# Kernel optimization log

Measured on AMD Instinct MI355X. Metric: run time of the kernel, lower is better.

## Reference

```python
import jax, jax.numpy as jnp
import numpy as np
import math

D = 2048
H = 32
HKV = 8
HD = D // H
ROPE_BASE = 10000.0


def _rope_cache(T, hd, base=ROPE_BASE):
    theta = 1.0 / base ** (jnp.arange(0, hd, 2, dtype=jnp.float32) / hd)  # [hd//2]
    t = jnp.arange(T, dtype=jnp.float32)
    freqs = t[:, None] * theta[None, :]  # [T, hd//2]
    return jnp.cos(freqs), jnp.sin(freqs)


def _apply_rope(x, cos, sin):
    # x: [B, H, T, HD]; interleaved-pair rotation
    B, Hh, T, hd = x.shape
    x_ = x.reshape(B, Hh, T, hd // 2, 2)
    x1, x2 = x_[..., 0], x_[..., 1]
    c = cos[None, None, :, :]
    s = sin[None, None, :, :]
    rx1 = x1 * c - x2 * s
    rx2 = x1 * s + x2 * c
    return jnp.stack([rx1, rx2], axis=-1).reshape(B, Hh, T, hd)


def setup_inputs() -> dict:
    key = jax.random.key(0)
    ks = jax.random.split(key, 5)
    B, T = 1, 2048
    sc = 0.02
    return {
        "x": jax.random.normal(ks[0], (B, T, D), dtype=jnp.float32),
        "wq": jax.random.normal(ks[1], (D, D), dtype=jnp.float32) * sc,
        "wk": jax.random.normal(ks[2], (HKV * HD, D), dtype=jnp.float32) * sc,
        "wv": jax.random.normal(ks[3], (HKV * HD, D), dtype=jnp.float32) * sc,
        "wo": jax.random.normal(ks[4], (D, D), dtype=jnp.float32) * sc,
    }


def reference(x, wq, wk, wv, wo):
    B, T, _ = x.shape
    q = (x @ wq.T).reshape(B, T, H, HD).transpose(0, 2, 1, 3)      # [B,H,T,HD]
    k = (x @ wk.T).reshape(B, T, HKV, HD).transpose(0, 2, 1, 3)    # [B,HKV,T,HD]
    v = (x @ wv.T).reshape(B, T, HKV, HD).transpose(0, 2, 1, 3)

    cos, sin = _rope_cache(T, HD)
    q = _apply_rope(q, cos, sin)
    k = _apply_rope(k, cos, sin)

    rep = H // HKV
    k = jnp.repeat(k, rep, axis=1)  # repeat_interleave over head dim
    v = jnp.repeat(v, rep, axis=1)

    scores = jnp.einsum("bhtd,bhsd->bhts", q, k) / math.sqrt(HD)
    mask = jnp.triu(jnp.full((T, T), -jnp.inf, dtype=scores.dtype), k=1)
    scores = scores + mask[None, None, :, :]
    attn = jax.nn.softmax(scores, axis=-1)

    y = jnp.einsum("bhts,bhsd->bhtd", attn, v)
    y = y.transpose(0, 2, 1, 3).reshape(B, T, D)
    return y @ wo.T
```

## Files before the change

### kernel.cpp

```cpp
#include <hip/hip_runtime.h>
#include <hip/hip_bf16.h>
#include <cstdint>
#include <cstddef>

#define TT 2048
#define DDIM 2048
#define NH 32
#define NKV 8
#define HDIM 64

typedef __attribute__((ext_vector_type(8))) short bf16x8;
typedef __attribute__((ext_vector_type(4))) float f32x4;
typedef __attribute__((ext_vector_type(16))) float f32x16;

__device__ __forceinline__ unsigned short f2bf(float f) {
  unsigned u = __float_as_uint(f);
  unsigned r = 0x7FFFu + ((u >> 16) & 1u);
  return (unsigned short)((u + r) >> 16);
}
__device__ __forceinline__ float bf2f(unsigned short u) {
  return __uint_as_float((unsigned)u << 16);
}

__device__ __forceinline__ void gl_lds16(const void* g, void* l) {
  __builtin_amdgcn_global_load_lds(
      (const __attribute__((address_space(1))) void*)g,
      (__attribute__((address_space(3))) void*)l, 16, 0, 0);
}

__device__ __forceinline__ unsigned pkbf(float lo, float hi) {
  unsigned r;
  asm("v_cvt_pk_bf16_f32 %0, %1, %2" : "=v"(r) : "v"(lo), "v"(hi));
  return r;
}
__device__ __forceinline__ void swap32(unsigned& dst, unsigned& src) {
  asm volatile("v_permlane32_swap_b32 %0, %1" : "+v"(dst), "+v"(src));
}
union W4 { unsigned w[4]; bf16x8 v; };

__global__ __launch_bounds__(256)
void cast5_kernel(const float* __restrict__ x, const float* __restrict__ wq,
                  const float* __restrict__ wk, const float* __restrict__ wv,
                  const float* __restrict__ wo,
                  unsigned short* __restrict__ xb, unsigned short* __restrict__ wqb,
                  unsigned short* __restrict__ wkb, unsigned short* __restrict__ wvb,
                  unsigned short* __restrict__ wob) {
  int i = blockIdx.x * 256 + threadIdx.x;
  const float* s; unsigned short* d; int off;
  if (i < 1048576)      { s = x;  d = xb;  off = i; }
  else if (i < 2097152) { s = wq; d = wqb; off = i - 1048576; }
  else if (i < 2359296) { s = wk; d = wkb; off = i - 2097152; }
  else if (i < 2621440) { s = wv; d = wvb; off = i - 2359296; }
  else                  { s = wo; d = wob; off = i - 2621440; }
  float4 f = reinterpret_cast<const float4*>(s)[off];
  ushort4 o;
  o.x = f2bf(f.x); o.y = f2bf(f.y); o.z = f2bf(f.z); o.w = f2bf(f.w);
  reinterpret_cast<ushort4*>(d)[off] = o;
}

__device__ __forceinline__ void gemm64_body(
    const unsigned short* __restrict__ A, const unsigned short* __restrict__ B,
    int K, size_t arow, size_t brow,
    unsigned short (*As)[64 * 64], unsigned short (*Bs)[128 * 64],
    f32x4 (&acc)[2][4]) {
  const int tid = threadIdx.x;
  const int wave = tid >> 6, lane = tid & 63;
  const int wm = wave >> 1, wn = wave & 1;
  const int lr = lane & 15;
  const int gb = lane >> 4;
  const int srow = lane >> 3;
  const int scol = (((lane & 7) ^ srow) << 3);

#define G64_STAGE(buf, k0)                                                       \
  {                                                                              \
    for (int i = 0; i < 2; ++i) {                                                \
      int blk = wave * 2 + i;                                                    \
      int r = blk * 8 + srow;                                                    \
      gl_lds16(A + arow + (size_t)r * K + (k0) + scol, &As[buf][blk * 8 * 64]);  \
    }                                                                            \
    for (int i = 0; i < 4; ++i) {                                                \
      int blk = wave * 4 + i;                                                    \
      int r = blk * 8 + srow;                                                    \
      gl_lds16(B + brow + (size_t)r * K + (k0) + scol, &Bs[buf][blk * 8 * 64]);  \
    }                                                                            \
  }

  const int nt = K >> 6;
  G64_STAGE(0, 0)
  __syncthreads();
  int cur = 0;
  for (int t = 0; t < nt; ++t) {
    if (t + 1 < nt) { G64_STAGE(cur ^ 1, (t + 1) << 6) }

    bf16x8 af[2][2], bfr[2][4];
    for (int mi = 0; mi < 2; ++mi) {
      int row = wm * 32 + mi * 16 + lr, sw = row & 7;
      af[0][mi] = *reinterpret_cast<const bf16x8*>(&As[cur][row * 64 + ((gb ^ sw) << 3)]);
      af[1][mi] = *reinterpret_cast<const bf16x8*>(&As[cur][row * 64 + (((4 + gb) ^ sw) << 3)]);
    }
    for (int ni = 0; ni < 4; ++ni) {
      int row = wn * 64 + ni * 16 + lr, sw = row & 7;
      bfr[0][ni] = *reinterpret_cast<const bf16x8*>(&Bs[cur][row * 64 + ((gb ^ sw) << 3)]);
      bfr[1][ni] = *reinterpret_cast<const bf16x8*>(&Bs[cur][row * 64 + (((4 + gb) ^ sw) << 3)]);
    }
    __builtin_amdgcn_s_setprio(1);
    for (int kk = 0; kk < 2; ++kk)
      for (int mi = 0; mi < 2; ++mi)
        for (int ni = 0; ni < 4; ++ni)
          acc[mi][ni] = __builtin_amdgcn_mfma_f32_16x16x32_bf16(af[kk][mi], bfr[kk][ni], acc[mi][ni], 0, 0, 0);
    __builtin_amdgcn_s_setprio(0);
    __syncthreads();
    cur ^= 1;
  }
#undef G64_STAGE
}

__global__ __launch_bounds__(256, 3)
void qkv_fused_kernel(const unsigned short* __restrict__ xb,
                      const unsigned short* __restrict__ wqb,
                      const unsigned short* __restrict__ wkb,
                      const unsigned short* __restrict__ wvb,
                      unsigned short* __restrict__ qhb,
                      unsigned short* __restrict__ khb,
                      unsigned short* __restrict__ vtb) {
  __shared__ __align__(16) unsigned short As[2][64 * 64];
  __shared__ __align__(16) unsigned short Bs[2][128 * 64];
  const int l = (int)(blockIdx.y * gridDim.x + blockIdx.x);
  const int nl = (l & 7) * 96 + (l >> 3);
  const int bx = nl & 31;
  const int bn = nl >> 5;

  const unsigned short* B; int n0, mode;
  if (bn < 16)      { B = wqb; n0 = bn;      mode = 0; }
  else if (bn < 20) { B = wkb; n0 = bn - 16; mode = 1; }
  else              { B = wvb; n0 = bn - 20; mode = 2; }

  f32x4 acc[2][4];
  for (int i = 0; i < 2; ++i)
    for (int j = 0; j < 4; ++j)
      acc[i][j] = (f32x4){0.f, 0.f, 0.f, 0.f};

  gemm64_body(xb, B, 2048, (size_t)(bx * 64) * 2048,
              (size_t)(n0 * 128) * 2048, As, Bs, acc);

  const int tid = threadIdx.x;
  const int wave = tid >> 6, lane = tid & 63;
  const int wm = wave >> 1, wn = wave & 1;
  const int lr = lane & 15;

  if (mode == 2) {
#pragma unroll
    for (int mi = 0; mi < 2; ++mi)
#pragma unroll
      for (int ni = 0; ni < 4; ++ni) {
        int n = n0 * 128 + wn * 64 + ni * 16 + lr;
        int tb = bx * 64 + wm * 32 + mi * 16 + (lane >> 4) * 4;
        ushort4 u;
        u.x = f2bf(acc[mi][ni][0]); u.y = f2bf(acc[mi][ni][1]);
        u.z = f2bf(acc[mi][ni][2]); u.w = f2bf(acc[mi][ni][3]);
        *reinterpret_cast<ushort4*>(&vtb[(size_t)n * TT + tb]) = u;
      }
  } else {
    unsigned short* dst = (mode == 0) ? qhb : khb;
    const float scale = (mode == 0) ? 0.125f : 1.0f;
#pragma unroll
    for (int mi = 0; mi < 2; ++mi)
#pragma unroll
      for (int ni = 0; ni < 4; ++ni) {
        int n = n0 * 128 + wn * 64 + ni * 16 + lr;
        int hh = n >> 6, d = n & 63, ii = d >> 1;
        float theta = exp2f(-(float)(2 * ii) * (13.287712379549449f / 64.0f));
        int tb = bx * 64 + wm * 32 + mi * 16 + (lane >> 4) * 4;
#pragma unroll
        for (int r = 0; r < 4; ++r) {
          float self = acc[mi][ni][r];
          float part = __shfl_xor(self, 1);
          float sn, cs;
          __sincosf((float)(tb + r) * theta, &sn, &cs);
          float val = (d & 1) ? (part * sn + self * cs) : (self * cs - part * sn);
          dst[((size_t)hh * TT + tb + r) * HDIM + d] = f2bf(val * scale);
        }
      }
  }
}

__global__ __launch_bounds__(256, 3)
void out_gemm_kernel(const unsigned short* __restrict__ yb,
                     const unsigned short* __restrict__ wob,
                     float* __restrict__ out) {
  __shared__ __align__(16) unsigned short As[2][64 * 64];
  __shared__ __align__(16) unsigned short Bs[2][128 * 64];
  const int l = (int)(blockIdx.y * gridDim.x + blockIdx.x);
  const int nl = (l & 7) * 64 + (l >> 3);
  const int bx = nl & 31;
  const int by = nl >> 5;

  f32x4 acc[2][4];
  for (int i = 0; i < 2; ++i)
    for (int j = 0; j < 4; ++j)
      acc[i][j] = (f32x4){0.f, 0.f, 0.f, 0.f};

  gemm64_body(yb, wob, 2048, (size_t)(bx * 64) * 2048,
              (size_t)(by * 128) * 2048, As, Bs, acc);

  const int tid = threadIdx.x;
  const int wave = tid >> 6, lane = tid & 63;
  const int wm = wave >> 1, wn = wave & 1;
  const int lr = lane & 15;
#pragma unroll
  for (int mi = 0; mi < 2; ++mi)
#pragma unroll
    for (int ni = 0; ni < 4; ++ni) {
      int col = by * 128 + wn * 64 + ni * 16 + lr;
      int rbase = bx * 64 + wm * 32 + mi * 16 + (lane >> 4) * 4;
#pragma unroll
      for (int r = 0; r < 4; ++r)
        out[(size_t)(rbase + r) * DDIM + col] = acc[mi][ni][r];
    }
}

__global__ __launch_bounds__(256)
void attn_kernel(const unsigned short* __restrict__ qh,
                 const unsigned short* __restrict__ kh,
                 const unsigned short* __restrict__ vt,
                 unsigned short* __restrict__ po,
                 float* __restrict__ pl) {
  __shared__ __align__(16) unsigned short Ks[2][64 * 64];
  __shared__ __align__(16) unsigned short Vts[2][64 * 64];
  const int kvg = blockIdx.x;
  const int by = blockIdx.y;
  const int qt = 63 - (by >> 1);
  const int par = by & 1;
  const int tid = threadIdx.x, wave = tid >> 6, lane = tid & 63;
  const int h = kvg * 4 + wave;
  const int qc = lane & 31, hi = lane >> 5;
  const int srow = lane >> 3;
  const int scol = (((lane & 7) ^ srow) << 3);

  bf16x8 qa[4];
  {
    const unsigned short* qrow = qh + ((size_t)h * TT + qt * 32 + qc) * HDIM + hi * 8;
#pragma unroll
    for (int ks = 0; ks < 4; ++ks)
      qa[ks] = *reinterpret_cast<const bf16x8*>(qrow + ks * 16);
  }

  f32x16 oA, oB;
#pragma unroll
  for (int r = 0; r < 16; ++r) { oA[r] = 0.f; oB[r] = 0.f; }
  float l_r = 0.f;

  const int njb = (qt >> 1) + 1;
  const int cnt = (njb - par + 1) >> 1;

#define A_STAGE(buf, jbx) do {                                                        \
    for (int i = 0; i < 2; ++i) {                                                     \
      int rblk = wave * 2 + i;                                                        \
      int rr = rblk * 8 + srow;                                                       \
      gl_lds16(kh + ((size_t)kvg * TT + (size_t)(jbx) * 64 + rr) * HDIM + scol,       \
               &Ks[buf][rblk * 8 * 64]);                                              \
      gl_lds16(vt + ((size_t)(kvg * HDIM + rr)) * TT + (size_t)(jbx) * 64 + scol,     \
               &Vts[buf][rblk * 8 * 64]);                                             \
    } } while (0)

  if (cnt > 0) {
    A_STAGE(0, par);
    __syncthreads();
    int cur = 0;

    for (int it = 0; it < cnt; ++it) {
      const int jb = par + 2 * it;
      if (it + 1 < cnt) A_STAGE(cur ^ 1, jb + 2);
      const bool diag = (jb == njb - 1);
      const bool hasB = (!diag) || (qt & 1);

      f32x16 stA, stB;
#pragma unroll
      for (int r = 0; r < 16; ++r) { stA[r] = 0.f; stB[r] = 0.f; }
      __builtin_amdgcn_s_setprio(1);
#pragma unroll
      for (int ks = 0; ks < 4; ++ks) {
        int row = qc, g = 2 * ks + hi;
        bf16x8 kf = *reinterpret_cast<const bf16x8*>(&Ks[cur][row * 64 + ((g ^ (row & 7)) << 3)]);
        stA = __builtin_amdgcn_mfma_f32_32x32x16_bf16(kf, qa[ks], stA, 0, 0, 0);
      }
      if (hasB) {
#pragma unroll
        for (int ks = 0; ks < 4; ++ks) {
          int row = 32 + qc, g = 2 * ks + hi;
          bf16x8 kf = *reinterpret_cast<const bf16x8*>(&Ks[cur][row * 64 + ((g ^ (row & 7)) << 3)]);
          stB = __builtin_amdgcn_mfma_f32_32x32x16_bf16(kf, qa[ks], stB, 0, 0, 0);
        }
      }
      __builtin_amdgcn_s_setprio(0);

      if (diag) {
        if (qt & 1) {
#pragma unroll
          for (int r = 0; r < 16; ++r) {
            int jloc = (r & 3) + 8 * (r >> 2) + 4 * hi;
            stB[r] = (jloc > qc) ? -1e30f : stB[r];
          }
        } else {
#pragma unroll
          for (int r = 0; r < 16; ++r) {
            int jloc = (r & 3) + 8 * (r >> 2) + 4 * hi;
            stA[r] = (jloc > qc) ? -1e30f : stA[r];
          }
        }
      }

#pragma unroll
      for (int r = 0; r < 16; ++r) { stA[r] = __expf(stA[r]); l_r += stA[r]; }
      if (hasB) {
#pragma unroll
        for (int r = 0; r < 16; ++r) { stB[r] = __expf(stB[r]); l_r += stB[r]; }
      }

      W4 pf0, pf1, pf2, pf3;
#define REPACK(F0, F1, S)                                                   \
      F0.w[0] = pkbf(S[0], S[1]);  F0.w[1] = pkbf(S[2], S[3]);              \
      F0.w[2] = pkbf(S[4], S[5]);  F0.w[3] = pkbf(S[6], S[7]);              \
      swap32(F0.w[0], F0.w[2]);    swap32(F0.w[1], F0.w[3]);                \
      F1.w[0] = pkbf(S[8], S[9]);  F1.w[1] = pkbf(S[10], S[11]);            \
      F1.w[2] = pkbf(S[12], S[13]); F1.w[3] = pkbf(S[14], S[15]);           \
      swap32(F1.w[0], F1.w[2]);    swap32(F1.w[1], F1.w[3]);
      REPACK(pf0, pf1, stA)
      if (hasB) { REPACK(pf2, pf3, stB) }
#undef REPACK

      {
        const unsigned short* Vb = &Vts[cur][0];
        int r0 = qc, r1 = 32 + qc;
        int s0 = r0 & 7, s1 = r1 & 7;
        bf16x8 b;
        __builtin_amdgcn_s_setprio(1);
        b = *reinterpret_cast<const bf16x8*>(Vb + r0 * 64 + (((0 + hi) ^ s0) << 3));
        oA = __builtin_amdgcn_mfma_f32_32x32x16_bf16(pf0.v, b, oA, 0, 0, 0);
        b = *reinterpret_cast<const bf16x8*>(Vb + r1 * 64 + (((0 + hi) ^ s1) << 3));
        oB = __builtin_amdgcn_mfma_f32_32x32x16_bf16(pf0.v, b, oB, 0, 0, 0);
        b = *reinterpret_cast<const bf16x8*>(Vb + r0 * 64 + (((2 + hi) ^ s0) << 3));
        oA = __builtin_amdgcn_mfma_f32_32x32x16_bf16(pf1.v, b, oA, 0, 0, 0);
        b = *reinterpret_cast<const bf16x8*>(Vb + r1 * 64 + (((2 + hi) ^ s1) << 3));
        oB = __builtin_amdgcn_mfma_f32_32x32x16_bf16(pf1.v, b, oB, 0, 0, 0);
        if (hasB) {
          b = *reinterpret_cast<const bf16x8*>(Vb + r0 * 64 + (((4 + hi) ^ s0) << 3));
          oA = __builtin_amdgcn_mfma_f32_32x32x16_bf16(pf2.v, b, oA, 0, 0, 0);
          b = *reinterpret_cast<const bf16x8*>(Vb + r1 * 64 + (((4 + hi) ^ s1) << 3));
          oB = __builtin_amdgcn_mfma_f32_32x32x16_bf16(pf2.v, b, oB, 0, 0, 0);
          b = *reinterpret_cast<const bf16x8*>(Vb + r0 * 64 + (((6 + hi) ^ s0) << 3));
          oA = __builtin_amdgcn_mfma_f32_32x32x16_bf16(pf3.v, b, oA, 0, 0, 0);
          b = *reinterpret_cast<const bf16x8*>(Vb + r1 * 64 + (((6 + hi) ^ s1) << 3));
          oB = __builtin_amdgcn_mfma_f32_32x32x16_bf16(pf3.v, b, oB, 0, 0, 0);
        }
        __builtin_amdgcn_s_setprio(0);
      }
      __syncthreads();
      cur ^= 1;
    }
  }
#undef A_STAGE

  l_r += __shfl_xor(l_r, 32);

  unsigned short* pop = po + (size_t)par * ((size_t)NH * TT * HDIM);
#pragma unroll
  for (int r = 0; r < 16; ++r) {
    int qrow = (r & 3) + 8 * (r >> 2) + 4 * hi;
    size_t base = ((size_t)h * TT + qt * 32 + qrow) * HDIM + qc;
    pop[base] = f2bf(oA[r]);
    pop[base + 32] = f2bf(oB[r]);
  }
  if (hi == 0) {
    size_t idx = ((size_t)par * NH + h) * TT + qt * 32 + qc;
    pl[idx] = l_r;
  }
}

__global__ __launch_bounds__(256)
void attn_merge_kernel(const unsigned short* __restrict__ po,
                       const float* __restrict__ pl,
                       unsigned short* __restrict__ y) {
  int idx = blockIdx.x * 256 + threadIdx.x;
  int row = idx >> 4;
  int d0 = (idx & 15) << 2;
  int h = row >> 11, t = row & (TT - 1);
  const size_t P = (size_t)NH * TT * HDIM;
  const int NT = NH * TT;

  float l0 = pl[row], l1 = pl[NT + row];
  ushort4 u0 = *reinterpret_cast<const ushort4*>(&po[(size_t)row * HDIM + d0]);
  ushort4 u1 = *reinterpret_cast<const ushort4*>(&po[P + (size_t)row * HDIM + d0]);
  float inv = 1.0f / (l0 + l1);
  ushort4 o;
  o.x = f2bf((bf2f(u0.x) + bf2f(u1.x)) * inv);
  o.y = f2bf((bf2f(u0.y) + bf2f(u1.y)) * inv);
  o.z = f2bf((bf2f(u0.z) + bf2f(u1.z)) * inv);
  o.w = f2bf((bf2f(u0.w) + bf2f(u1.w)) * inv);
  *reinterpret_cast<ushort4*>(&y[(size_t)t * DDIM + h * HDIM + d0]) = o;
}

extern "C" void kernel_launch(void* const* d_in, const int* in_sizes, int n_in,
                              void* d_out, int out_size, void* d_ws, size_t ws_size,
                              hipStream_t stream) {
  const float* x  = (const float*)d_in[0];
  const float* wq = (const float*)d_in[1];
  const float* wk = (const float*)d_in[2];
  const float* wv = (const float*)d_in[3];
  const float* wo = (const float*)d_in[4];
  float* out = (float*)d_out;
  char* ws = (char*)d_ws;

  unsigned short* xb  = (unsigned short*)(ws + (size_t)0);
  unsigned short* wqb = (unsigned short*)(ws + ((size_t)8  << 20));
  unsigned short* wkb = (unsigned short*)(ws + ((size_t)16 << 20));
  unsigned short* wvb = (unsigned short*)(ws + ((size_t)18 << 20));
  unsigned short* wob = (unsigned short*)(ws + ((size_t)20 << 20));
  unsigned short* po  = (unsigned short*)(ws + ((size_t)28 << 20));
  float*          pl  = (float*)(ws + ((size_t)45 << 20));
  unsigned short* qhb = (unsigned short*)(ws + ((size_t)52 << 20));
  unsigned short* khb = (unsigned short*)(ws + ((size_t)60 << 20));
  unsigned short* vtb = (unsigned short*)(ws + ((size_t)62 << 20));
  unsigned short* yb  = (unsigned short*)(ws + ((size_t)64 << 20));

  cast5_kernel<<<14336, 256, 0, stream>>>(x, wq, wk, wv, wo, xb, wqb, wkb, wvb, wob);

  qkv_fused_kernel<<<dim3(32, 24), 256, 0, stream>>>(xb, wqb, wkb, wvb, qhb, khb, vtb);

  attn_kernel<<<dim3(8, 128), 256, 0, stream>>>(qhb, khb, vtb, po, pl);
  attn_merge_kernel<<<4096, 256, 0, stream>>>(po, pl, yb);

  out_gemm_kernel<<<dim3(32, 16), 256, 0, stream>>>(yb, wob, out);
}
```

Measured before the change: 115.6 us.

## Fuse weight fp32-to-bf16 conversion into GEMM B-tile loading

The weight casts are removed from the standalone cast pass. The GEMMs now load fp32 weight tiles into registers, convert them to bf16 with packed conversion instructions, and store them to LDS after the MFMA work, so the next tile is still prefetched. This drops the separate write and re-read of the bf16 weights. In exchange, each GEMM block re-reads fp32 weights at twice the bytes (each B tile is read by 32 row-blocks), and register pressure rises from the staged float4s.

```diff
diff --git a/kernel.cpp b/kernel.cpp
--- a/kernel.cpp
+++ b/kernel.cpp
@@ -39,27 +39,16 @@
 union W4 { unsigned w[4]; bf16x8 v; };
 
 __global__ __launch_bounds__(256)
-void cast5_kernel(const float* __restrict__ x, const float* __restrict__ wq,
-                  const float* __restrict__ wk, const float* __restrict__ wv,
-                  const float* __restrict__ wo,
-                  unsigned short* __restrict__ xb, unsigned short* __restrict__ wqb,
-                  unsigned short* __restrict__ wkb, unsigned short* __restrict__ wvb,
-                  unsigned short* __restrict__ wob) {
+void cast_x_kernel(const float* __restrict__ x, unsigned short* __restrict__ xb) {
   int i = blockIdx.x * 256 + threadIdx.x;
-  const float* s; unsigned short* d; int off;
-  if (i < 1048576)      { s = x;  d = xb;  off = i; }
-  else if (i < 2097152) { s = wq; d = wqb; off = i - 1048576; }
-  else if (i < 2359296) { s = wk; d = wkb; off = i - 2097152; }
-  else if (i < 2621440) { s = wv; d = wvb; off = i - 2359296; }
-  else                  { s = wo; d = wob; off = i - 2621440; }
-  float4 f = reinterpret_cast<const float4*>(s)[off];
+  float4 f = reinterpret_cast<const float4*>(x)[i];
   ushort4 o;
   o.x = f2bf(f.x); o.y = f2bf(f.y); o.z = f2bf(f.z); o.w = f2bf(f.w);
-  reinterpret_cast<ushort4*>(d)[off] = o;
-}
-
-__device__ __forceinline__ void gemm64_body(
-    const unsigned short* __restrict__ A, const unsigned short* __restrict__ B,
+  reinterpret_cast<ushort4*>(xb)[i] = o;
+}
+
+__device__ __forceinline__ void gemm64f_body(
+    const unsigned short* __restrict__ A, const float* __restrict__ B,
     int K, size_t arow, size_t brow,
     unsigned short (*As)[64 * 64], unsigned short (*Bs)[128 * 64],
     f32x4 (&acc)[2][4]) {
@@ -70,27 +59,44 @@
   const int gb = lane >> 4;
   const int srow = lane >> 3;
   const int scol = (((lane & 7) ^ srow) << 3);
-
-#define G64_STAGE(buf, k0)                                                       \
-  {                                                                              \
-    for (int i = 0; i < 2; ++i) {                                                \
-      int blk = wave * 2 + i;                                                    \
-      int r = blk * 8 + srow;                                                    \
-      gl_lds16(A + arow + (size_t)r * K + (k0) + scol, &As[buf][blk * 8 * 64]);  \
-    }                                                                            \
-    for (int i = 0; i < 4; ++i) {                                                \
-      int blk = wave * 4 + i;                                                    \
-      int r = blk * 8 + srow;                                                    \
-      gl_lds16(B + brow + (size_t)r * K + (k0) + scol, &Bs[buf][blk * 8 * 64]);  \
-    }                                                                            \
+  const int bcol = (lane & 7) << 3;
+  const int bdst = srow * 64 + scol;
+
+  float4 breg[4][2];
+
+#define A_STG(buf, k0)                                                         \
+  for (int i = 0; i < 2; ++i) {                                                \
+    int blk = wave * 2 + i;                                                    \
+    int r = blk * 8 + srow;                                                    \
+    gl_lds16(A + arow + (size_t)r * K + (k0) + scol, &As[buf][blk * 8 * 64]);  \
+  }
+#define B_LOAD(k0)                                                             \
+  for (int i = 0; i < 4; ++i) {                                                \
+    int blk = wave * 4 + i;                                                    \
+    int r = blk * 8 + srow;                                                    \
+    const float* p = B + brow + (size_t)r * K + (k0) + bcol;                   \
+    breg[i][0] = *reinterpret_cast<const float4*>(p);                          \
+    breg[i][1] = *reinterpret_cast<const float4*>(p + 4);                      \
+  }
+#define B_STORE(buf)                                                           \
+  for (int i = 0; i < 4; ++i) {                                                \
+    int blk = wave * 4 + i;                                                    \
+    W4 w;                                                                      \
+    w.w[0] = pkbf(breg[i][0].x, breg[i][0].y);                                 \
+    w.w[1] = pkbf(breg[i][0].z, breg[i][0].w);                                 \
+    w.w[2] = pkbf(breg[i][1].x, breg[i][1].y);                                 \
+    w.w[3] = pkbf(breg[i][1].z, breg[i][1].w);                                 \
+    *reinterpret_cast<bf16x8*>(&Bs[buf][blk * 512 + bdst]) = w.v;              \
   }
 
   const int nt = K >> 6;
-  G64_STAGE(0, 0)
+  B_LOAD(0)
+  A_STG(0, 0)
+  B_STORE(0)
   __syncthreads();
   int cur = 0;
   for (int t = 0; t < nt; ++t) {
-    if (t + 1 < nt) { G64_STAGE(cur ^ 1, (t + 1) << 6) }
+    if (t + 1 < nt) { B_LOAD((t + 1) << 6) A_STG(cur ^ 1, (t + 1) << 6) }
 
     bf16x8 af[2][2], bfr[2][4];
     for (int mi = 0; mi < 2; ++mi) {
@@ -109,17 +115,20 @@
         for (int ni = 0; ni < 4; ++ni)
           acc[mi][ni] = __builtin_amdgcn_mfma_f32_16x16x32_bf16(af[kk][mi], bfr[kk][ni], acc[mi][ni], 0, 0, 0);
     __builtin_amdgcn_s_setprio(0);
+    if (t + 1 < nt) { B_STORE(cur ^ 1) }
     __syncthreads();
     cur ^= 1;
   }
-#undef G64_STAGE
+#undef A_STG
+#undef B_LOAD
+#undef B_STORE
 }
 
 __global__ __launch_bounds__(256, 3)
 void qkv_fused_kernel(const unsigned short* __restrict__ xb,
-                      const unsigned short* __restrict__ wqb,
-                      const unsigned short* __restrict__ wkb,
-                      const unsigned short* __restrict__ wvb,
+                      const float* __restrict__ wq,
+                      const float* __restrict__ wk,
+                      const float* __restrict__ wv,
                       unsigned short* __restrict__ qhb,
                       unsigned short* __restrict__ khb,
                       unsigned short* __restrict__ vtb) {
@@ -130,18 +139,18 @@
   const int bx = nl & 31;
   const int bn = nl >> 5;
 
-  const unsigned short* B; int n0, mode;
-  if (bn < 16)      { B = wqb; n0 = bn;      mode = 0; }
-  else if (bn < 20) { B = wkb; n0 = bn - 16; mode = 1; }
-  else              { B = wvb; n0 = bn - 20; mode = 2; }
+  const float* B; int n0, mode;
+  if (bn < 16)      { B = wq; n0 = bn;      mode = 0; }
+  else if (bn < 20) { B = wk; n0 = bn - 16; mode = 1; }
+  else              { B = wv; n0 = bn - 20; mode = 2; }
 
   f32x4 acc[2][4];
   for (int i = 0; i < 2; ++i)
     for (int j = 0; j < 4; ++j)
       acc[i][j] = (f32x4){0.f, 0.f, 0.f, 0.f};
 
-  gemm64_body(xb, B, 2048, (size_t)(bx * 64) * 2048,
-              (size_t)(n0 * 128) * 2048, As, Bs, acc);
+  gemm64f_body(xb, B, 2048, (size_t)(bx * 64) * 2048,
+               (size_t)(n0 * 128) * 2048, As, Bs, acc);
 
   const int tid = threadIdx.x;
   const int wave = tid >> 6, lane = tid & 63;
@@ -186,7 +195,7 @@
 
 __global__ __launch_bounds__(256, 3)
 void out_gemm_kernel(const unsigned short* __restrict__ yb,
-                     const unsigned short* __restrict__ wob,
+                     const float* __restrict__ wo,
                      float* __restrict__ out) {
   __shared__ __align__(16) unsigned short As[2][64 * 64];
   __shared__ __align__(16) unsigned short Bs[2][128 * 64];
@@ -200,8 +209,8 @@
     for (int j = 0; j < 4; ++j)
       acc[i][j] = (f32x4){0.f, 0.f, 0.f, 0.f};
 
-  gemm64_body(yb, wob, 2048, (size_t)(bx * 64) * 2048,
-              (size_t)(by * 128) * 2048, As, Bs, acc);
+  gemm64f_body(yb, wo, 2048, (size_t)(bx * 64) * 2048,
+               (size_t)(by * 128) * 2048, As, Bs, acc);
 
   const int tid = threadIdx.x;
   const int wave = tid >> 6, lane = tid & 63;
@@ -412,10 +421,6 @@
   char* ws = (char*)d_ws;
 
   unsigned short* xb  = (unsigned short*)(ws + (size_t)0);
-  unsigned short* wqb = (unsigned short*)(ws + ((size_t)8  << 20));
-  unsigned short* wkb = (unsigned short*)(ws + ((size_t)16 << 20));
-  unsigned short* wvb = (unsigned short*)(ws + ((size_t)18 << 20));
-  unsigned short* wob = (unsigned short*)(ws + ((size_t)20 << 20));
   unsigned short* po  = (unsigned short*)(ws + ((size_t)28 << 20));
   float*          pl  = (float*)(ws + ((size_t)45 << 20));
   unsigned short* qhb = (unsigned short*)(ws + ((size_t)52 << 20));
@@ -423,12 +428,12 @@
   unsigned short* vtb = (unsigned short*)(ws + ((size_t)62 << 20));
   unsigned short* yb  = (unsigned short*)(ws + ((size_t)64 << 20));
 
-  cast5_kernel<<<14336, 256, 0, stream>>>(x, wq, wk, wv, wo, xb, wqb, wkb, wvb, wob);
-
-  qkv_fused_kernel<<<dim3(32, 24), 256, 0, stream>>>(xb, wqb, wkb, wvb, qhb, khb, vtb);
+  cast_x_kernel<<<4096, 256, 0, stream>>>(x, xb);
+
+  qkv_fused_kernel<<<dim3(32, 24), 256, 0, stream>>>(xb, wq, wk, wv, qhb, khb, vtb);
 
   attn_kernel<<<dim3(8, 128), 256, 0, stream>>>(qhb, khb, vtb, po, pl);
   attn_merge_kernel<<<4096, 256, 0, stream>>>(po, pl, yb);
 
-  out_gemm_kernel<<<dim3(32, 16), 256, 0, stream>>>(yb, wob, out);
-}
+  out_gemm_kernel<<<dim3(32, 16), 256, 0, stream>>>(yb, wo, out);
+}
```

Measured after the change: 130.4 us. 1.13x slower.
